# Kernel optimization log

Measured on AMD Instinct MI355X. Metric: run time of the kernel, lower is better.

Reference implementation:

```python
import jax, jax.numpy as jnp
import numpy as np

NMS_THRESH = 0.5
SCORE_THRESH = 0.2
MAX_SUBJECT = 15
MAX_OBJECT = 15
B, NS, NO = 32, 512, 512


def _make_boxes(k, b, n):
    u = jax.random.uniform(k, (b, n, 4))
    xy = u[..., :2] * 1000.0          # top-left corner
    wh = u[..., 2:] * 200.0 + 1.0     # positive width/height
    return jnp.concatenate([xy, xy + wh], axis=-1)  # valid xyxy boxes


def setup_inputs() -> dict:
    key = jax.random.key(0)
    ks = jax.random.split(key, 6)
    return {
        "subj_boxes": _make_boxes(ks[0], B, NS),
        "subj_scores": jax.random.uniform(ks[1], (B, NS)),
        "subj_labels": jax.random.randint(ks[2], (B, NS), 0, 30, dtype=jnp.int32),
        "obj_boxes": _make_boxes(ks[3], B, NO),
        "obj_scores": jax.random.uniform(ks[4], (B, NO)),
        "obj_labels": jax.random.randint(ks[5], (B, NO), 0, 30, dtype=jnp.int32),
    }


def reference(subj_boxes, subj_scores, subj_labels, obj_boxes, obj_scores, obj_labels):
    # concat subject + object detections per image, as in preprocess()
    boxes = jnp.concatenate([subj_boxes, obj_boxes], axis=1)    # [B,N,4]
    scores = jnp.concatenate([subj_scores, obj_scores], axis=1) # [B,N]
    labels = jnp.concatenate([subj_labels, obj_labels], axis=1) # [B,N]
    b, n = scores.shape
    is_subj = jnp.arange(n) < subj_boxes.shape[1]               # [N]

    # sort by score descending (matches the argsort after NMS; greedy NMS
    # preserves this ordering among survivors)
    order = jnp.argsort(-scores, axis=1)
    boxes = jnp.take_along_axis(boxes, order[..., None], axis=1)
    scores = jnp.take_along_axis(scores, order, axis=1)
    labels = jnp.take_along_axis(labels, order, axis=1)
    is_subj = jnp.take(is_subj, order)                          # [B,N]

    active = scores >= SCORE_THRESH

    # torchvision batched_nms: offset boxes per class so distinct classes
    # never overlap (comparisons only -> no gradient path)
    max_coord = jax.lax.stop_gradient(jnp.max(boxes))
    ob = boxes + labels.astype(boxes.dtype)[..., None] * (max_coord + 1.0)

    # pairwise IoU [B,N,N]
    area = (ob[..., 2] - ob[..., 0]) * (ob[..., 3] - ob[..., 1])
    lt = jnp.maximum(ob[:, :, None, :2], ob[:, None, :, :2])
    rb = jnp.minimum(ob[:, :, None, 2:], ob[:, None, :, 2:])
    wh = jnp.clip(rb - lt, 0.0)
    inter = wh[..., 0] * wh[..., 1]
    iou = inter / (area[:, :, None] + area[:, None, :] - inter)

    later = jnp.arange(n)[None, :] > jnp.arange(n)[:, None]     # strictly lower-score

    def body(i, suppressed):  # greedy NMS, vectorized over batch
        keep_i = active[:, i] & ~suppressed[:, i]
        return suppressed | (keep_i[:, None] & (iou[:, i, :] > NMS_THRESH) & later[i])

    suppressed = jax.lax.fori_loop(0, n, body, jnp.zeros((b, n), dtype=bool))
    kept = active & ~suppressed

    # split survivors into subjects / objects, keep top max_subject/max_object
    neg = jnp.finfo(scores.dtype).min
    sub_key = jnp.where(kept & is_subj, scores, neg)
    obj_key = jnp.where(kept & ~is_subj, scores, neg)
    sv, si = jax.lax.top_k(sub_key, MAX_SUBJECT)
    ov, oi = jax.lax.top_k(obj_key, MAX_OBJECT)
    idx = jnp.concatenate([si, oi], axis=1)                     # [B,K]
    valid = jnp.concatenate([sv, ov], axis=1) > neg             # [B,K]

    out_boxes = jnp.take_along_axis(boxes, idx[..., None], axis=1) * valid[..., None]
    out_scores = jnp.take_along_axis(scores, idx, axis=1) * valid
    out_labels = jnp.where(valid, jnp.take_along_axis(labels, idx, axis=1), -1)
    num_subjects = jnp.sum(sv > neg, axis=1)
    return out_boxes, out_scores, out_labels, num_subjects, valid
```

## Files before the change

### kernel.cpp

```cpp
#include <hip/hip_runtime.h>
#include <stdint.h>

#define BQ    32
#define NSUB  512
#define NDET  1024
#define NCLS  30
#define KSLOT 30
#define BCAP  96

#pragma clang fp contract(off)

typedef unsigned long long u64;

__global__ __launch_bounds__(512) void bucket_kernel(
    const float* __restrict__ sb, const float* __restrict__ ss,
    const int*   __restrict__ sl,
    const float* __restrict__ ob, const float* __restrict__ os,
    const int*   __restrict__ ol,
    float* __restrict__ pmax, int* __restrict__ cnts,
    u64* __restrict__ bkeys, float4* __restrict__ bboxes)
{
    const int b = blockIdx.x, t = threadIdx.x;
    const int lane = t & 63, w = t >> 6;
    __shared__ int   lcnt[NCLS];
    __shared__ float wred[8];

    if (t < NCLS) lcnt[t] = 0;

    float4 bxs = *(const float4*)(sb + (size_t)(b * NSUB + t) * 4);
    float4 bxo = *(const float4*)(ob + (size_t)(b * NSUB + t) * 4);
    float scs = ss[b * NSUB + t];  int lbs = sl[b * NSUB + t];
    float sco = os[b * NSUB + t];  int lbo = ol[b * NSUB + t];

    float m = fmaxf(fmaxf(fmaxf(bxs.x, bxs.y), fmaxf(bxs.z, bxs.w)),
                    fmaxf(fmaxf(bxo.x, bxo.y), fmaxf(bxo.z, bxo.w)));
    for (int off = 32; off; off >>= 1) m = fmaxf(m, __shfl_xor(m, off));
    if (lane == 0) wred[w] = m;
    __syncthreads();
    if (t == 0) {
        float mm = wred[0];
        for (int i = 1; i < 8; ++i) mm = fmaxf(mm, wred[i]);
        pmax[b] = mm;
    }

    if (scs >= 0.2f) {
        int pos = atomicAdd(&lcnt[lbs], 1);
        if (pos < BCAP) {
            size_t s = ((size_t)b * NCLS + lbs) * BCAP + pos;
            bkeys[s]  = ((u64)__float_as_uint(scs) << 32) | (u64)(1023 - t);
            bboxes[s] = bxs;
        }
    }
    if (sco >= 0.2f) {
        int pos = atomicAdd(&lcnt[lbo], 1);
        if (pos < BCAP) {
            size_t s = ((size_t)b * NCLS + lbo) * BCAP + pos;
            bkeys[s]  = ((u64)__float_as_uint(sco) << 32) | (u64)(1023 - (512 + t));
            bboxes[s] = bxo;
        }
    }
    __syncthreads();
    if (t < NCLS) {
        int c = lcnt[t];
        cnts[b * NCLS + t] = (c < BCAP) ? c : BCAP;
    }
}

__global__ __launch_bounds__(64) void nms_class_kernel(
    const float* __restrict__ pmax, const int* __restrict__ cnts,
    const u64* __restrict__ bkeys, const float4* __restrict__ bboxes,
    u64* __restrict__ subk, u64* __restrict__ objk,
    float4* __restrict__ subb, float4* __restrict__ objb)
{
#pragma clang fp contract(off)
    const int c    = blockIdx.x;
    const int b    = blockIdx.y;
    const int lane = threadIdx.x;

    __shared__ u64    keyarr[BCAP];
    __shared__ u64    skey[BCAP];
    __shared__ float4 bxs4[BCAP];

    const size_t base = (size_t)b * NCLS + c;

    u64    K1 = bkeys[base * BCAP + lane];
    float4 B1 = bboxes[base * BCAP + lane];
    u64 K2 = 0; float4 B2 = make_float4(0.f, 0.f, 0.f, 0.f);
    if (lane < BCAP - 64) {
        K2 = bkeys[base * BCAP + 64 + lane];
        B2 = bboxes[base * BCAP + 64 + lane];
    }
    const int cnt = cnts[base];
    float pv = pmax[lane & 31];
    for (int off = 32; off; off >>= 1) pv = fmaxf(pv, __shfl_xor(pv, off));
    const float mco  = pv + 1.0f;
    const float offc = (float)c * mco;

    keyarr[lane] = K1;
    if (lane < BCAP - 64) keyarr[64 + lane] = K2;
    __threadfence_block();

    {
        int r = 0;
        for (int l = 0; l < cnt; ++l) r += (keyarr[l] > K1) ? 1 : 0;
        if (lane < cnt) { skey[r] = K1; bxs4[r] = B1; }
    }
    if (cnt > 64) {
        int e = 64 + lane;
        int r = 0;
        for (int l = 0; l < cnt; ++l) r += (keyarr[l] > K2) ? 1 : 0;
        if (e < cnt) { skey[r] = K2; bxs4[r] = B2; }
    }
    __threadfence_block();

    const int  lim1  = (cnt < 64) ? cnt : 64;
    const bool have1 = (lane < lim1);
    u64 SK1 = have1 ? skey[lane] : 0;
    int idx1 = 1023 - (int)(unsigned)(SK1 & 0xffffffffull);
    float4 bj1 = have1 ? bxs4[lane] : make_float4(0.f, 0.f, 0.f, 0.f);
    const bool have2 = (64 + lane) < cnt;
    u64 SK2 = 0; int idx2 = 0; float4 bj2 = make_float4(0.f, 0.f, 0.f, 0.f);
    if (cnt > 64) {
        SK2 = have2 ? skey[64 + lane] : 0;
        idx2 = 1023 - (int)(unsigned)(SK2 & 0xffffffffull);
        if (have2) bj2 = bxs4[64 + lane];
    }

    float j0 = bj1.x + offc, j1 = bj1.y + offc;
    float j2v = bj1.z + offc, j3 = bj1.w + offc;
    float aj = (j2v - j0) * (j3 - j1);
    u64 ov = 0;
    for (int l = 0; l < lim1; ++l) {
        float4 bl = bxs4[l];
        float i0 = bl.x + offc, i1 = bl.y + offc;
        float i2 = bl.z + offc, i3 = bl.w + offc;
        float ai = (i2 - i0) * (i3 - i1);
        if (have1 && l < lane) {
            float ltx = fmaxf(i0, j0), lty = fmaxf(i1, j1);
            float rbx = fminf(i2, j2v), rby = fminf(i3, j3);
            float wx = fmaxf(rbx - ltx, 0.0f), wy = fmaxf(rby - lty, 0.0f);
            float inter = wx * wy;
            float iou = inter / ((ai + aj) - inter);
            if (iou > 0.5f) ov |= (1ull << l);
        }
    }
    bool sup1 = !have1;
    for (int l = 0; l < lim1; ++l) {
        u64 bal = __ballot(sup1);
        if (!((bal >> l) & 1ull)) sup1 = sup1 || (((ov >> l) & 1ull) != 0ull);
    }
    const bool kept1 = have1 && !sup1;
    const u64 keptA = __ballot(kept1);

    bool kept2 = false;
    if (cnt > 64) {
        float k0 = bj2.x + offc, k1 = bj2.y + offc;
        float k2 = bj2.z + offc, k3 = bj2.w + offc;
        float ak = (k2 - k0) * (k3 - k1);
        bool sup2 = !have2;
        for (int l = 0; l < 64; ++l) {
            if ((keptA >> l) & 1ull) {
                float4 bl = bxs4[l];
                float i0 = bl.x + offc, i1 = bl.y + offc;
                float i2 = bl.z + offc, i3 = bl.w + offc;
                float ai = (i2 - i0) * (i3 - i1);
                if (!sup2) {
                    float ltx = fmaxf(i0, k0), lty = fmaxf(i1, k1);
                    float rbx = fminf(i2, k2), rby = fminf(i3, k3);
                    float wx = fmaxf(rbx - ltx, 0.0f), wy = fmaxf(rby - lty, 0.0f);
                    float inter = wx * wy;
                    float iou = inter / ((ai + ak) - inter);
                    if (iou > 0.5f) sup2 = true;
                }
            }
        }
        u64 ov2 = 0;
        const int lim2 = cnt - 64;
        for (int l = 0; l < lim2; ++l) {
            float4 bl = bxs4[64 + l];
            float i0 = bl.x + offc, i1 = bl.y + offc;
            float i2 = bl.z + offc, i3 = bl.w + offc;
            float ai = (i2 - i0) * (i3 - i1);
            if (have2 && l < lane) {
                float ltx = fmaxf(i0, k0), lty = fmaxf(i1, k1);
                float rbx = fminf(i2, k2), rby = fminf(i3, k3);
                float wx = fmaxf(rbx - ltx, 0.0f), wy = fmaxf(rby - lty, 0.0f);
                float inter = wx * wy;
                float iou = inter / ((ai + ak) - inter);
                if (iou > 0.5f) ov2 |= (1ull << l);
            }
        }
        for (int l = 0; l < lim2; ++l) {
            u64 bal = __ballot(sup2);
            if (!((bal >> l) & 1ull)) sup2 = sup2 || (((ov2 >> l) & 1ull) != 0ull);
        }
        kept2 = have2 && !sup2;
    }

    const bool s1 = kept1 && (idx1 < NSUB), o1 = kept1 && (idx1 >= NSUB);
    const bool s2 = kept2 && (idx2 < NSUB), o2 = kept2 && (idx2 >= NSUB);
    const u64 mS1 = __ballot(s1), mS2 = __ballot(s2);
    const u64 mO1 = __ballot(o1), mO2 = __ballot(o2);
    const u64 ltm = (1ull << lane) - 1ull;
    u64*    subp = subk + base * 15;   float4* sbbp = subb + base * 15;
    u64*    objp = objk + base * 15;   float4* obbp = objb + base * 15;
    if (s1) { int p = (int)__popcll(mS1 & ltm); if (p < 15) { subp[p] = SK1; sbbp[p] = bj1; } }
    if (s2) { int p = (int)__popcll(mS1) + (int)__popcll(mS2 & ltm); if (p < 15) { subp[p] = SK2; sbbp[p] = bj2; } }
    if (o1) { int p = (int)__popcll(mO1 & ltm); if (p < 15) { objp[p] = SK1; obbp[p] = bj1; } }
    if (o2) { int p = (int)__popcll(mO1) + (int)__popcll(mO2 & ltm); if (p < 15) { objp[p] = SK2; obbp[p] = bj2; } }
    int tS = (int)(__popcll(mS1) + __popcll(mS2)); if (tS > 15) tS = 15;
    int tO = (int)(__popcll(mO1) + __popcll(mO2)); if (tO > 15) tO = 15;
    if (lane >= tS && lane < 15) subp[lane] = 0;
    if (lane >= tO && lane < 15) objp[lane] = 0;
}

__global__ __launch_bounds__(64) void select_kernel(
    const u64* __restrict__ subk, const u64* __restrict__ objk,
    const float4* __restrict__ subb, const float4* __restrict__ objb,
    float* __restrict__ out)
{
    const int b    = blockIdx.x;
    const int side = blockIdx.y;
    const int lane = threadIdx.x;

    float* outB = out;
    float* outS = out + BQ * KSLOT * 4;
    float* outL = outS + BQ * KSLOT;
    float* outN = outL + BQ * KSLOT;
    float* outV = outN + BQ;

    const u64*    src  = (side ? objk : subk) + (size_t)b * NCLS * 15;
    const float4* srcb = (side ? objb : subb) + (size_t)b * NCLS * 15;

    __shared__ float4 sbx[NCLS * 15];

    u64 kk[8];
    #pragma unroll
    for (int i = 0; i < 8; ++i) {
        int p = lane + 64 * i;
        kk[i] = (p < NCLS * 15) ? src[p] : 0;
    }
    for (int p = lane; p < NCLS * 15; p += 64) sbx[p] = srcb[p];
    __threadfence_block();

    int nvalid = 0;
    for (int r = 0; r < 15; ++r) {
        u64 lm = 0;
        #pragma unroll
        for (int i = 0; i < 8; ++i) lm = (kk[i] > lm) ? kk[i] : lm;
        u64 gm = lm;
        for (int off = 32; off; off >>= 1) {
            u64 o = __shfl_xor(gm, off);
            if (o > gm) gm = o;
        }
        int p = b * KSLOT + (side ? (15 + r) : r);
        if (gm == 0) {
            if (lane == 0) {
                *(float4*)(outB + (size_t)p * 4) = make_float4(0.f, 0.f, 0.f, 0.f);
                outS[p] = 0.0f; outL[p] = -1.0f; outV[p] = 0.0f;
            }
        } else {
            u64 win = __ballot(lm == gm);
            int wl = (int)__ffsll(win) - 1;
            if (lane == wl) {
                int sp = 0;
                #pragma unroll
                for (int i = 0; i < 8; ++i) if (kk[i] == gm) sp = lane + 64 * i;
                #pragma unroll
                for (int i = 0; i < 8; ++i) if (kk[i] == gm) kk[i] = 0;
                float4 bx = sbx[sp];
                float score = __uint_as_float((unsigned)(gm >> 32));
                int cls = sp / 15;
                *(float4*)(outB + (size_t)p * 4) = bx;
                outS[p] = score;
                outL[p] = (float)cls;
                outV[p] = 1.0f;
            }
            nvalid++;
        }
    }
    if (side == 0 && lane == 0) outN[b] = (float)nvalid;
}

extern "C" void kernel_launch(void* const* d_in, const int* in_sizes, int n_in,
                              void* d_out, int out_size, void* d_ws, size_t ws_size,
                              hipStream_t stream) {
    const float* sb = (const float*)d_in[0];
    const float* ss = (const float*)d_in[1];
    const int*   sl = (const int*)d_in[2];
    const float* ob = (const float*)d_in[3];
    const float* os = (const float*)d_in[4];
    const int*   ol = (const int*)d_in[5];

    float*  pmax   = (float*)d_ws;
    int*    cnts   = (int*)((char*)d_ws + 256);
    u64*    bkeys  = (u64*)((char*)d_ws + 8192);
    float4* bboxes = (float4*)((char*)d_ws + 745472);
    u64*    subk   = (u64*)((char*)d_ws + 2220032);
    u64*    objk   = subk + (size_t)BQ * NCLS * 15;
    float4* subb   = (float4*)((char*)d_ws + 2450432);
    float4* objb   = subb + (size_t)BQ * NCLS * 15;

    bucket_kernel<<<dim3(BQ), dim3(512), 0, stream>>>(
        sb, ss, sl, ob, os, ol, pmax, cnts, bkeys, bboxes);
    nms_class_kernel<<<dim3(NCLS, BQ), dim3(64), 0, stream>>>(
        pmax, cnts, bkeys, bboxes, subk, objk, subb, objb);
    select_kernel<<<dim3(BQ, 2), dim3(64), 0, stream>>>(
        subk, objk, subb, objb, (float*)d_out);
}
```

Before: 86.85 us.

## Fuse bucketing into per-class NMS and merge selection via last-block atomic

Moves class bucketing out of a separate kernel. Each per-class NMS block now reads all 1024 detections of its image and compacts the matching ones with ballot and popcount, which also makes the bucket order deterministic. The final top-15 selection is folded into the last block per image to finish, using an atomic counter and threadfences, so a kernel launch and the global bucket round-trip are removed. In exchange, every block re-reads the full image input (30x redundant global loads), and one block per image does serial selection work for both sides.

```diff
diff --git a/kernel.cpp b/kernel.cpp
--- a/kernel.cpp
+++ b/kernel.cpp
@@ -12,28 +12,19 @@
 
 typedef unsigned long long u64;
 
-__global__ __launch_bounds__(512) void bucket_kernel(
-    const float* __restrict__ sb, const float* __restrict__ ss,
-    const int*   __restrict__ sl,
-    const float* __restrict__ ob, const float* __restrict__ os,
-    const int*   __restrict__ ol,
-    float* __restrict__ pmax, int* __restrict__ cnts,
-    u64* __restrict__ bkeys, float4* __restrict__ bboxes)
+__global__ __launch_bounds__(512) void pmax_kernel(
+    const float* __restrict__ sb, const float* __restrict__ ob,
+    float* __restrict__ pmax, int* __restrict__ done)
 {
     const int b = blockIdx.x, t = threadIdx.x;
     const int lane = t & 63, w = t >> 6;
-    __shared__ int   lcnt[NCLS];
     __shared__ float wred[8];
-
-    if (t < NCLS) lcnt[t] = 0;
-
-    float4 bxs = *(const float4*)(sb + (size_t)(b * NSUB + t) * 4);
-    float4 bxo = *(const float4*)(ob + (size_t)(b * NSUB + t) * 4);
-    float scs = ss[b * NSUB + t];  int lbs = sl[b * NSUB + t];
-    float sco = os[b * NSUB + t];  int lbo = ol[b * NSUB + t];
-
-    float m = fmaxf(fmaxf(fmaxf(bxs.x, bxs.y), fmaxf(bxs.z, bxs.w)),
-                    fmaxf(fmaxf(bxo.x, bxo.y), fmaxf(bxo.z, bxo.w)));
+    const float4* sb4 = (const float4*)sb;
+    const float4* ob4 = (const float4*)ob;
+    float4 a  = sb4[(size_t)b * NSUB + t];
+    float4 c4 = ob4[(size_t)b * NSUB + t];
+    float m = fmaxf(fmaxf(fmaxf(a.x, a.y), fmaxf(a.z, a.w)),
+                    fmaxf(fmaxf(c4.x, c4.y), fmaxf(c4.z, c4.w)));
     for (int off = 32; off; off >>= 1) m = fmaxf(m, __shfl_xor(m, off));
     if (lane == 0) wred[w] = m;
     __syncthreads();
@@ -41,75 +32,87 @@
         float mm = wred[0];
         for (int i = 1; i < 8; ++i) mm = fmaxf(mm, wred[i]);
         pmax[b] = mm;
-    }
-
-    if (scs >= 0.2f) {
-        int pos = atomicAdd(&lcnt[lbs], 1);
-        if (pos < BCAP) {
-            size_t s = ((size_t)b * NCLS + lbs) * BCAP + pos;
-            bkeys[s]  = ((u64)__float_as_uint(scs) << 32) | (u64)(1023 - t);
-            bboxes[s] = bxs;
-        }
-    }
-    if (sco >= 0.2f) {
-        int pos = atomicAdd(&lcnt[lbo], 1);
-        if (pos < BCAP) {
-            size_t s = ((size_t)b * NCLS + lbo) * BCAP + pos;
-            bkeys[s]  = ((u64)__float_as_uint(sco) << 32) | (u64)(1023 - (512 + t));
-            bboxes[s] = bxo;
-        }
-    }
-    __syncthreads();
-    if (t < NCLS) {
-        int c = lcnt[t];
-        cnts[b * NCLS + t] = (c < BCAP) ? c : BCAP;
+        done[b] = 0;
     }
 }
 
-__global__ __launch_bounds__(64) void nms_class_kernel(
-    const float* __restrict__ pmax, const int* __restrict__ cnts,
-    const u64* __restrict__ bkeys, const float4* __restrict__ bboxes,
+__global__ __launch_bounds__(64) void nms_fused_kernel(
+    const float* __restrict__ sb, const float* __restrict__ ss,
+    const int*   __restrict__ sl,
+    const float* __restrict__ ob, const float* __restrict__ os,
+    const int*   __restrict__ ol,
+    const float* __restrict__ pmax, int* __restrict__ done,
     u64* __restrict__ subk, u64* __restrict__ objk,
-    float4* __restrict__ subb, float4* __restrict__ objb)
+    float4* __restrict__ subb, float4* __restrict__ objb,
+    float* __restrict__ out)
 {
 #pragma clang fp contract(off)
     const int c    = blockIdx.x;
     const int b    = blockIdx.y;
     const int lane = threadIdx.x;
 
-    __shared__ u64    keyarr[BCAP];
+    __shared__ u64    ukey[BCAP];
+    __shared__ float4 ubox[BCAP];
     __shared__ u64    skey[BCAP];
-    __shared__ float4 bxs4[BCAP];
-
-    const size_t base = (size_t)b * NCLS + c;
-
-    u64    K1 = bkeys[base * BCAP + lane];
-    float4 B1 = bboxes[base * BCAP + lane];
-    u64 K2 = 0; float4 B2 = make_float4(0.f, 0.f, 0.f, 0.f);
-    if (lane < BCAP - 64) {
-        K2 = bkeys[base * BCAP + 64 + lane];
-        B2 = bboxes[base * BCAP + 64 + lane];
-    }
-    const int cnt = cnts[base];
+    __shared__ float4 sbox[BCAP];
+    __shared__ float4 selbx[NCLS * 15];
+
+    const float4* sb4 = (const float4*)sb;
+    const float4* ob4 = (const float4*)ob;
+
     float pv = pmax[lane & 31];
     for (int off = 32; off; off >>= 1) pv = fmaxf(pv, __shfl_xor(pv, off));
     const float mco  = pv + 1.0f;
     const float offc = (float)c * mco;
 
-    keyarr[lane] = K1;
-    if (lane < BCAP - 64) keyarr[64 + lane] = K2;
+    float4 rbx[16]; float rsc[16]; int rlb[16];
+    #pragma unroll
+    for (int it = 0; it < 16; ++it) {
+        int i = it * 64 + lane;
+        if (it < 8) {
+            rbx[it] = sb4[(size_t)b * NSUB + i];
+            rsc[it] = ss[b * NSUB + i];
+            rlb[it] = sl[b * NSUB + i];
+        } else {
+            int j = i - NSUB;
+            rbx[it] = ob4[(size_t)b * NSUB + j];
+            rsc[it] = os[b * NSUB + j];
+            rlb[it] = ol[b * NSUB + j];
+        }
+    }
+    int cbase = 0;
+    #pragma unroll
+    for (int it = 0; it < 16; ++it) {
+        int i = it * 64 + lane;
+        bool match = (rsc[it] >= 0.2f) && (rlb[it] == c);
+        u64 bal = __ballot(match);
+        if (match) {
+            int pos = cbase + (int)__popcll(bal & ((1ull << lane) - 1ull));
+            if (pos < BCAP) {
+                ukey[pos] = ((u64)__float_as_uint(rsc[it]) << 32) | (u64)(1023 - i);
+                ubox[pos] = rbx[it];
+            }
+        }
+        cbase += (int)__popcll(bal);
+    }
+    const int cnt = (cbase < BCAP) ? cbase : BCAP;
     __threadfence_block();
+
+    u64    K1 = ukey[lane];
+    float4 B1 = ubox[lane];
+    u64 K2 = 0; float4 B2 = make_float4(0.f, 0.f, 0.f, 0.f);
+    if (lane < BCAP - 64) { K2 = ukey[64 + lane]; B2 = ubox[64 + lane]; }
 
     {
         int r = 0;
-        for (int l = 0; l < cnt; ++l) r += (keyarr[l] > K1) ? 1 : 0;
-        if (lane < cnt) { skey[r] = K1; bxs4[r] = B1; }
+        for (int l = 0; l < cnt; ++l) r += (ukey[l] > K1) ? 1 : 0;
+        if (lane < cnt) { skey[r] = K1; sbox[r] = B1; }
     }
     if (cnt > 64) {
         int e = 64 + lane;
         int r = 0;
-        for (int l = 0; l < cnt; ++l) r += (keyarr[l] > K2) ? 1 : 0;
-        if (e < cnt) { skey[r] = K2; bxs4[r] = B2; }
+        for (int l = 0; l < cnt; ++l) r += (ukey[l] > K2) ? 1 : 0;
+        if (e < cnt) { skey[r] = K2; sbox[r] = B2; }
     }
     __threadfence_block();
 
@@ -117,13 +120,13 @@
     const bool have1 = (lane < lim1);
     u64 SK1 = have1 ? skey[lane] : 0;
     int idx1 = 1023 - (int)(unsigned)(SK1 & 0xffffffffull);
-    float4 bj1 = have1 ? bxs4[lane] : make_float4(0.f, 0.f, 0.f, 0.f);
+    float4 bj1 = have1 ? sbox[lane] : make_float4(0.f, 0.f, 0.f, 0.f);
     const bool have2 = (64 + lane) < cnt;
     u64 SK2 = 0; int idx2 = 0; float4 bj2 = make_float4(0.f, 0.f, 0.f, 0.f);
     if (cnt > 64) {
         SK2 = have2 ? skey[64 + lane] : 0;
         idx2 = 1023 - (int)(unsigned)(SK2 & 0xffffffffull);
-        if (have2) bj2 = bxs4[64 + lane];
+        if (have2) bj2 = sbox[64 + lane];
     }
 
     float j0 = bj1.x + offc, j1 = bj1.y + offc;
@@ -131,14 +134,14 @@
     float aj = (j2v - j0) * (j3 - j1);
     u64 ov = 0;
     for (int l = 0; l < lim1; ++l) {
-        float4 bl = bxs4[l];
+        float4 bl = sbox[l];
         float i0 = bl.x + offc, i1 = bl.y + offc;
         float i2 = bl.z + offc, i3 = bl.w + offc;
         float ai = (i2 - i0) * (i3 - i1);
         if (have1 && l < lane) {
             float ltx = fmaxf(i0, j0), lty = fmaxf(i1, j1);
-            float rbx = fminf(i2, j2v), rby = fminf(i3, j3);
-            float wx = fmaxf(rbx - ltx, 0.0f), wy = fmaxf(rby - lty, 0.0f);
+            float rbx_ = fminf(i2, j2v), rby = fminf(i3, j3);
+            float wx = fmaxf(rbx_ - ltx, 0.0f), wy = fmaxf(rby - lty, 0.0f);
             float inter = wx * wy;
             float iou = inter / ((ai + aj) - inter);
             if (iou > 0.5f) ov |= (1ull << l);
@@ -160,14 +163,14 @@
         bool sup2 = !have2;
         for (int l = 0; l < 64; ++l) {
             if ((keptA >> l) & 1ull) {
-                float4 bl = bxs4[l];
+                float4 bl = sbox[l];
                 float i0 = bl.x + offc, i1 = bl.y + offc;
                 float i2 = bl.z + offc, i3 = bl.w + offc;
                 float ai = (i2 - i0) * (i3 - i1);
                 if (!sup2) {
                     float ltx = fmaxf(i0, k0), lty = fmaxf(i1, k1);
-                    float rbx = fminf(i2, k2), rby = fminf(i3, k3);
-                    float wx = fmaxf(rbx - ltx, 0.0f), wy = fmaxf(rby - lty, 0.0f);
+                    float rbx_ = fminf(i2, k2), rby = fminf(i3, k3);
+                    float wx = fmaxf(rbx_ - ltx, 0.0f), wy = fmaxf(rby - lty, 0.0f);
                     float inter = wx * wy;
                     float iou = inter / ((ai + ak) - inter);
                     if (iou > 0.5f) sup2 = true;
@@ -177,14 +180,14 @@
         u64 ov2 = 0;
         const int lim2 = cnt - 64;
         for (int l = 0; l < lim2; ++l) {
-            float4 bl = bxs4[64 + l];
+            float4 bl = sbox[64 + l];
             float i0 = bl.x + offc, i1 = bl.y + offc;
             float i2 = bl.z + offc, i3 = bl.w + offc;
             float ai = (i2 - i0) * (i3 - i1);
             if (have2 && l < lane) {
                 float ltx = fmaxf(i0, k0), lty = fmaxf(i1, k1);
-                float rbx = fminf(i2, k2), rby = fminf(i3, k3);
-                float wx = fmaxf(rbx - ltx, 0.0f), wy = fmaxf(rby - lty, 0.0f);
+                float rbx_ = fminf(i2, k2), rby = fminf(i3, k3);
+                float wx = fmaxf(rbx_ - ltx, 0.0f), wy = fmaxf(rby - lty, 0.0f);
                 float inter = wx * wy;
                 float iou = inter / ((ai + ak) - inter);
                 if (iou > 0.5f) ov2 |= (1ull << l);
@@ -197,6 +200,7 @@
         kept2 = have2 && !sup2;
     }
 
+    const size_t base = (size_t)b * NCLS + c;
     const bool s1 = kept1 && (idx1 < NSUB), o1 = kept1 && (idx1 >= NSUB);
     const bool s2 = kept2 && (idx2 < NSUB), o2 = kept2 && (idx2 >= NSUB);
     const u64 mS1 = __ballot(s1), mS2 = __ballot(s2);
@@ -212,16 +216,13 @@
     int tO = (int)(__popcll(mO1) + __popcll(mO2)); if (tO > 15) tO = 15;
     if (lane >= tS && lane < 15) subp[lane] = 0;
     if (lane >= tO && lane < 15) objp[lane] = 0;
-}
-
-__global__ __launch_bounds__(64) void select_kernel(
-    const u64* __restrict__ subk, const u64* __restrict__ objk,
-    const float4* __restrict__ subb, const float4* __restrict__ objb,
-    float* __restrict__ out)
-{
-    const int b    = blockIdx.x;
-    const int side = blockIdx.y;
-    const int lane = threadIdx.x;
+
+    __threadfence();
+    int prev = 0;
+    if (lane == 0) prev = atomicAdd(&done[b], 1);
+    prev = __shfl(prev, 0);
+    if (prev != NCLS - 1) return;
+    __threadfence();
 
     float* outB = out;
     float* outS = out + BQ * KSLOT * 4;
@@ -229,57 +230,58 @@
     float* outN = outL + BQ * KSLOT;
     float* outV = outN + BQ;
 
-    const u64*    src  = (side ? objk : subk) + (size_t)b * NCLS * 15;
-    const float4* srcb = (side ? objb : subb) + (size_t)b * NCLS * 15;
-
-    __shared__ float4 sbx[NCLS * 15];
-
-    u64 kk[8];
-    #pragma unroll
-    for (int i = 0; i < 8; ++i) {
-        int p = lane + 64 * i;
-        kk[i] = (p < NCLS * 15) ? src[p] : 0;
-    }
-    for (int p = lane; p < NCLS * 15; p += 64) sbx[p] = srcb[p];
-    __threadfence_block();
-
-    int nvalid = 0;
-    for (int r = 0; r < 15; ++r) {
-        u64 lm = 0;
+    for (int side = 0; side < 2; ++side) {
+        const u64*    src  = (side ? objk : subk) + (size_t)b * NCLS * 15;
+        const float4* srcb = (side ? objb : subb) + (size_t)b * NCLS * 15;
+
+        u64 kk[8];
         #pragma unroll
-        for (int i = 0; i < 8; ++i) lm = (kk[i] > lm) ? kk[i] : lm;
-        u64 gm = lm;
-        for (int off = 32; off; off >>= 1) {
-            u64 o = __shfl_xor(gm, off);
-            if (o > gm) gm = o;
-        }
-        int p = b * KSLOT + (side ? (15 + r) : r);
-        if (gm == 0) {
-            if (lane == 0) {
-                *(float4*)(outB + (size_t)p * 4) = make_float4(0.f, 0.f, 0.f, 0.f);
-                outS[p] = 0.0f; outL[p] = -1.0f; outV[p] = 0.0f;
-            }
-        } else {
-            u64 win = __ballot(lm == gm);
-            int wl = (int)__ffsll(win) - 1;
-            if (lane == wl) {
-                int sp = 0;
-                #pragma unroll
-                for (int i = 0; i < 8; ++i) if (kk[i] == gm) sp = lane + 64 * i;
-                #pragma unroll
-                for (int i = 0; i < 8; ++i) if (kk[i] == gm) kk[i] = 0;
-                float4 bx = sbx[sp];
-                float score = __uint_as_float((unsigned)(gm >> 32));
-                int cls = sp / 15;
-                *(float4*)(outB + (size_t)p * 4) = bx;
-                outS[p] = score;
-                outL[p] = (float)cls;
-                outV[p] = 1.0f;
-            }
-            nvalid++;
-        }
-    }
-    if (side == 0 && lane == 0) outN[b] = (float)nvalid;
+        for (int i = 0; i < 8; ++i) {
+            int p = lane + 64 * i;
+            kk[i] = (p < NCLS * 15) ? src[p] : 0;
+        }
+        for (int p = lane; p < NCLS * 15; p += 64) selbx[p] = srcb[p];
+        __threadfence_block();
+
+        int nvalid = 0;
+        for (int r = 0; r < 15; ++r) {
+            u64 lm = 0;
+            #pragma unroll
+            for (int i = 0; i < 8; ++i) lm = (kk[i] > lm) ? kk[i] : lm;
+            u64 gm = lm;
+            for (int off = 32; off; off >>= 1) {
+                u64 o = __shfl_xor(gm, off);
+                if (o > gm) gm = o;
+            }
+            int p = b * KSLOT + (side ? (15 + r) : r);
+            if (gm == 0) {
+                if (lane == 0) {
+                    *(float4*)(outB + (size_t)p * 4) = make_float4(0.f, 0.f, 0.f, 0.f);
+                    outS[p] = 0.0f; outL[p] = -1.0f; outV[p] = 0.0f;
+                }
+            } else {
+                u64 win = __ballot(lm == gm);
+                int wl = (int)__ffsll(win) - 1;
+                if (lane == wl) {
+                    int sp = 0;
+                    #pragma unroll
+                    for (int i = 0; i < 8; ++i) if (kk[i] == gm) sp = lane + 64 * i;
+                    #pragma unroll
+                    for (int i = 0; i < 8; ++i) if (kk[i] == gm) kk[i] = 0;
+                    float4 bx = selbx[sp];
+                    float score = __uint_as_float((unsigned)(gm >> 32));
+                    int cls = sp / 15;
+                    *(float4*)(outB + (size_t)p * 4) = bx;
+                    outS[p] = score;
+                    outL[p] = (float)cls;
+                    outV[p] = 1.0f;
+                }
+                nvalid++;
+            }
+        }
+        if (side == 0 && lane == 0) outN[b] = (float)nvalid;
+        __threadfence_block();
+    }
 }
 
 extern "C" void kernel_launch(void* const* d_in, const int* in_sizes, int n_in,
@@ -292,19 +294,15 @@
     const float* os = (const float*)d_in[4];
     const int*   ol = (const int*)d_in[5];
 
-    float*  pmax   = (float*)d_ws;
-    int*    cnts   = (int*)((char*)d_ws + 256);
-    u64*    bkeys  = (u64*)((char*)d_ws + 8192);
-    float4* bboxes = (float4*)((char*)d_ws + 745472);
-    u64*    subk   = (u64*)((char*)d_ws + 2220032);
-    u64*    objk   = subk + (size_t)BQ * NCLS * 15;
-    float4* subb   = (float4*)((char*)d_ws + 2450432);
-    float4* objb   = subb + (size_t)BQ * NCLS * 15;
-
-    bucket_kernel<<<dim3(BQ), dim3(512), 0, stream>>>(
-        sb, ss, sl, ob, os, ol, pmax, cnts, bkeys, bboxes);
-    nms_class_kernel<<<dim3(NCLS, BQ), dim3(64), 0, stream>>>(
-        pmax, cnts, bkeys, bboxes, subk, objk, subb, objb);
-    select_kernel<<<dim3(BQ, 2), dim3(64), 0, stream>>>(
-        subk, objk, subb, objb, (float*)d_out);
+    float*  pmax = (float*)d_ws;
+    int*    done = (int*)((char*)d_ws + 256);
+    u64*    subk = (u64*)((char*)d_ws + 4096);
+    u64*    objk = (u64*)((char*)d_ws + 119296);
+    float4* subb = (float4*)((char*)d_ws + 234496);
+    float4* objb = (float4*)((char*)d_ws + 464896);
+
+    pmax_kernel<<<dim3(BQ), dim3(512), 0, stream>>>(sb, ob, pmax, done);
+    nms_fused_kernel<<<dim3(NCLS, BQ), dim3(64), 0, stream>>>(
+        sb, ss, sl, ob, os, ol, pmax, done, subk, objk, subb, objb,
+        (float*)d_out);
 }
```

After: 116.5 us. +34.2%, slower.

## Skip decided boxes in per-class NMS and rank-sort top-15 in parallel select

Applied to the files above, without the earlier changes.

Each per-class NMS wave now resolves greedy suppression by jumping to the next undecided box with ffs and one ballot per kept box, instead of ballotting once per candidate. Cross-tile suppression loops only over kept boxes through bit iteration. The select kernel drops the 15 serial wave-wide max reductions: it compacts the nonzero keys into shared memory with an atomic counter and ranks each key by counting larger keys, using 512 threads. This cuts serial ballot and reduction chains, at the cost of an O(n^2) rank count and atomics in shared memory.

```diff
diff --git a/kernel.cpp b/kernel.cpp
--- a/kernel.cpp
+++ b/kernel.cpp
@@ -144,12 +144,17 @@
             if (iou > 0.5f) ov |= (1ull << l);
         }
     }
-    bool sup1 = !have1;
-    for (int l = 0; l < lim1; ++l) {
-        u64 bal = __ballot(sup1);
-        if (!((bal >> l) & 1ull)) sup1 = sup1 || (((ov >> l) & 1ull) != 0ull);
-    }
-    const bool kept1 = have1 && !sup1;
+    u64 keptm = 0;
+    {
+        u64 undec = __ballot(have1);
+        while (undec) {
+            int l = (int)__ffsll((unsigned long long)undec) - 1;
+            keptm |= (1ull << l);
+            u64 supby = __ballot(((ov >> l) & 1ull) != 0ull);
+            undec &= ~(supby | (1ull << l));
+        }
+    }
+    const bool kept1 = have1 && ((keptm >> lane) & 1ull);
     const u64 keptA = __ballot(kept1);
 
     bool kept2 = false;
@@ -158,20 +163,21 @@
         float k2 = bj2.z + offc, k3 = bj2.w + offc;
         float ak = (k2 - k0) * (k3 - k1);
         bool sup2 = !have2;
-        for (int l = 0; l < 64; ++l) {
-            if ((keptA >> l) & 1ull) {
-                float4 bl = bxs4[l];
-                float i0 = bl.x + offc, i1 = bl.y + offc;
-                float i2 = bl.z + offc, i3 = bl.w + offc;
-                float ai = (i2 - i0) * (i3 - i1);
-                if (!sup2) {
-                    float ltx = fmaxf(i0, k0), lty = fmaxf(i1, k1);
-                    float rbx = fminf(i2, k2), rby = fminf(i3, k3);
-                    float wx = fmaxf(rbx - ltx, 0.0f), wy = fmaxf(rby - lty, 0.0f);
-                    float inter = wx * wy;
-                    float iou = inter / ((ai + ak) - inter);
-                    if (iou > 0.5f) sup2 = true;
-                }
+        u64 ka = keptA;
+        while (ka) {
+            int l = (int)__ffsll((unsigned long long)ka) - 1;
+            ka &= ka - 1ull;
+            float4 bl = bxs4[l];
+            float i0 = bl.x + offc, i1 = bl.y + offc;
+            float i2 = bl.z + offc, i3 = bl.w + offc;
+            float ai = (i2 - i0) * (i3 - i1);
+            if (!sup2) {
+                float ltx = fmaxf(i0, k0), lty = fmaxf(i1, k1);
+                float rbx = fminf(i2, k2), rby = fminf(i3, k3);
+                float wx = fmaxf(rbx - ltx, 0.0f), wy = fmaxf(rby - lty, 0.0f);
+                float inter = wx * wy;
+                float iou = inter / ((ai + ak) - inter);
+                if (iou > 0.5f) sup2 = true;
             }
         }
         u64 ov2 = 0;
@@ -190,11 +196,15 @@
                 if (iou > 0.5f) ov2 |= (1ull << l);
             }
         }
-        for (int l = 0; l < lim2; ++l) {
-            u64 bal = __ballot(sup2);
-            if (!((bal >> l) & 1ull)) sup2 = sup2 || (((ov2 >> l) & 1ull) != 0ull);
-        }
-        kept2 = have2 && !sup2;
+        u64 keptm2 = 0;
+        u64 undec2 = __ballot(have2 && !sup2);
+        while (undec2) {
+            int l = (int)__ffsll((unsigned long long)undec2) - 1;
+            keptm2 |= (1ull << l);
+            u64 supby = __ballot(((ov2 >> l) & 1ull) != 0ull);
+            undec2 &= ~(supby | (1ull << l));
+        }
+        kept2 = have2 && !sup2 && ((keptm2 >> lane) & 1ull);
     }
 
     const bool s1 = kept1 && (idx1 < NSUB), o1 = kept1 && (idx1 >= NSUB);
@@ -214,14 +224,15 @@
     if (lane >= tO && lane < 15) objp[lane] = 0;
 }
 
-__global__ __launch_bounds__(64) void select_kernel(
+__global__ __launch_bounds__(512) void select_kernel(
     const u64* __restrict__ subk, const u64* __restrict__ objk,
     const float4* __restrict__ subb, const float4* __restrict__ objb,
     float* __restrict__ out)
 {
     const int b    = blockIdx.x;
     const int side = blockIdx.y;
-    const int lane = threadIdx.x;
+    const int t    = threadIdx.x;
+    const int N    = NCLS * 15;
 
     float* outB = out;
     float* outS = out + BQ * KSLOT * 4;
@@ -229,57 +240,41 @@
     float* outN = outL + BQ * KSLOT;
     float* outV = outN + BQ;
 
-    const u64*    src  = (side ? objk : subk) + (size_t)b * NCLS * 15;
-    const float4* srcb = (side ? objb : subb) + (size_t)b * NCLS * 15;
-
-    __shared__ float4 sbx[NCLS * 15];
-
-    u64 kk[8];
-    #pragma unroll
-    for (int i = 0; i < 8; ++i) {
-        int p = lane + 64 * i;
-        kk[i] = (p < NCLS * 15) ? src[p] : 0;
-    }
-    for (int p = lane; p < NCLS * 15; p += 64) sbx[p] = srcb[p];
-    __threadfence_block();
-
-    int nvalid = 0;
-    for (int r = 0; r < 15; ++r) {
-        u64 lm = 0;
-        #pragma unroll
-        for (int i = 0; i < 8; ++i) lm = (kk[i] > lm) ? kk[i] : lm;
-        u64 gm = lm;
-        for (int off = 32; off; off >>= 1) {
-            u64 o = __shfl_xor(gm, off);
-            if (o > gm) gm = o;
-        }
-        int p = b * KSLOT + (side ? (15 + r) : r);
-        if (gm == 0) {
-            if (lane == 0) {
-                *(float4*)(outB + (size_t)p * 4) = make_float4(0.f, 0.f, 0.f, 0.f);
-                outS[p] = 0.0f; outL[p] = -1.0f; outV[p] = 0.0f;
-            }
-        } else {
-            u64 win = __ballot(lm == gm);
-            int wl = (int)__ffsll(win) - 1;
-            if (lane == wl) {
-                int sp = 0;
-                #pragma unroll
-                for (int i = 0; i < 8; ++i) if (kk[i] == gm) sp = lane + 64 * i;
-                #pragma unroll
-                for (int i = 0; i < 8; ++i) if (kk[i] == gm) kk[i] = 0;
-                float4 bx = sbx[sp];
-                float score = __uint_as_float((unsigned)(gm >> 32));
-                int cls = sp / 15;
-                *(float4*)(outB + (size_t)p * 4) = bx;
-                outS[p] = score;
-                outL[p] = (float)cls;
-                outV[p] = 1.0f;
-            }
-            nvalid++;
-        }
-    }
-    if (side == 0 && lane == 0) outN[b] = (float)nvalid;
+    const u64*    src  = (side ? objk : subk) + (size_t)b * N;
+    const float4* srcb = (side ? objb : subb) + (size_t)b * N;
+
+    __shared__ u64 ckey[N + 64];
+    __shared__ int cntv;
+
+    if (t == 0) cntv = 0;
+    __syncthreads();
+
+    u64 k = (t < N) ? src[t] : 0;
+    int pos = -1;
+    if (k != 0) pos = atomicAdd(&cntv, 1);
+    if (pos >= 0) ckey[pos] = k;
+    __syncthreads();
+    const int nv  = cntv;
+    const int nvc = (nv < 15) ? nv : 15;
+
+    if (pos >= 0) {
+        int rank = 0;
+        for (int l = 0; l < nv; ++l) rank += (ckey[l] > k) ? 1 : 0;
+        if (rank < 15) {
+            int p = b * KSLOT + (side ? (15 + rank) : rank);
+            float4 bx = srcb[t];
+            *(float4*)(outB + (size_t)p * 4) = bx;
+            outS[p] = __uint_as_float((unsigned)(k >> 32));
+            outL[p] = (float)(t / 15);
+            outV[p] = 1.0f;
+        }
+    }
+    if (t >= nvc && t < 15) {
+        int p = b * KSLOT + (side ? (15 + t) : t);
+        *(float4*)(outB + (size_t)p * 4) = make_float4(0.f, 0.f, 0.f, 0.f);
+        outS[p] = 0.0f; outL[p] = -1.0f; outV[p] = 0.0f;
+    }
+    if (side == 0 && t == 0) outN[b] = (float)nvc;
 }
 
 extern "C" void kernel_launch(void* const* d_in, const int* in_sizes, int n_in,
@@ -305,6 +300,6 @@
         sb, ss, sl, ob, os, ol, pmax, cnts, bkeys, bboxes);
     nms_class_kernel<<<dim3(NCLS, BQ), dim3(64), 0, stream>>>(
         pmax, cnts, bkeys, bboxes, subk, objk, subb, objb);
-    select_kernel<<<dim3(BQ, 2), dim3(64), 0, stream>>>(
+    select_kernel<<<dim3(BQ, 2), dim3(512), 0, stream>>>(
         subk, objk, subb, objb, (float*)d_out);
 }
```

After: 82.28 us, median of 2. 1.06x faster.
